# Optimization experiments

Hardware: AMD Instinct MI355X
Metric: run time of the kernel (lower is better)

The kernel has to match this reference:

```python
import jax, jax.numpy as jnp
import numpy as np

B, TX, TY, C, H = 2, 1024, 4096, 768, 12
D = C // H  # head_dim = 64


def setup_inputs() -> dict:
    key = jax.random.key(0)
    ks = jax.random.split(key, 7)
    x = jax.random.normal(ks[0], (B, TX, C), dtype=jnp.float32)
    y = jax.random.normal(ks[1], (B, TY, C), dtype=jnp.float32)
    # sorted float timestamps in [0, TY]
    x_t = jnp.sort(jax.random.uniform(ks[2], (B, TX), dtype=jnp.float32) * TY, axis=-1)
    y_t = jnp.sort(jax.random.uniform(ks[3], (B, TY), dtype=jnp.float32) * TY, axis=-1)
    y_t = y_t.at[:, 0].set(0.0)  # guarantee every query sees >=1 valid key
    Wq = jax.random.normal(ks[4], (C, C), dtype=jnp.float32) * 0.02
    Wkv = jax.random.normal(ks[5], (C, 2 * C), dtype=jnp.float32) * 0.02
    Wproj = jax.random.normal(ks[6], (C, C), dtype=jnp.float32) * 0.02
    # RotaryEmbedding(dim=D, learned_freq=True): init values are the standard inv freqs
    inv_freq = 1.0 / (10000.0 ** (jnp.arange(0, D, 2, dtype=jnp.float32) / D))
    return {"x": x, "x_t": x_t, "y": y, "y_t": y_t, "dist": 512, "min_dist": 0,
            "Wq": Wq, "Wkv": Wkv, "Wproj": Wproj, "inv_freq": inv_freq}


def _rotate_half(t):
    # interleaved pair rotation: (x1, x2) -> (-x2, x1)
    p = t.reshape(t.shape[:-1] + (-1, 2))
    x1, x2 = p[..., 0], p[..., 1]
    return jnp.stack((-x2, x1), axis=-1).reshape(t.shape)


def _apply_rope(t, pos, inv_freq):
    # t: (B,H,T,D), pos: (B,T), inv_freq: (D/2,)
    f = pos[:, None, :, None] * inv_freq          # (B,1,T,D/2)
    f = jnp.repeat(f, 2, axis=-1)                 # (B,1,T,D) interleaved
    return t * jnp.cos(f) + _rotate_half(t) * jnp.sin(f)


def reference(x, x_t, y, y_t, dist, min_dist, Wq, Wkv, Wproj, inv_freq):
    q = (x @ Wq).reshape(B, TX, H, D).transpose(0, 2, 1, 3)   # (B,H,TX,D)
    kv = y @ Wkv
    k = kv[..., :C].reshape(B, TY, H, D).transpose(0, 2, 1, 3)
    v = kv[..., C:].reshape(B, TY, H, D).transpose(0, 2, 1, 3)
    q = _apply_rope(q, x_t, inv_freq)
    k = _apply_rope(k, y_t, inv_freq)
    # time-window mask: valid iff (x_t - min_dist) >= y_t and (x_t - min_dist) <= y_t + dist
    xt = (x_t - min_dist)[:, :, None]             # (B,TX,1)
    yt = y_t[:, None, :]                          # (B,1,TY)
    mask = (xt >= yt) & (xt <= yt + dist)         # (B,TX,TY)
    scores = jnp.einsum('bhqd,bhkd->bhqk', q, k) / jnp.sqrt(jnp.float32(D))
    scores = jnp.where(mask[:, None, :, :], scores, -jnp.inf)
    attn = jax.nn.softmax(scores, axis=-1)
    out = jnp.einsum('bhqk,bhkd->bhqd', attn, v)
    out = out.transpose(0, 2, 1, 3).reshape(B, TX, C)
    return out @ Wproj
```

## Files before the change

### kernel.cpp

```cpp
#include <hip/hip_runtime.h>
#include <hip/hip_bf16.h>
#include <math.h>

#define B_ 2
#define TX_ 1024
#define TY_ 4096
#define C_ 768
#define H_ 12
#define D_ 64
#define NSPLIT 4
#define R_ (B_ * H_ * TX_)

typedef __bf16 bf16x8 __attribute__((ext_vector_type(8)));
typedef float floatx4 __attribute__((ext_vector_type(4)));

__device__ __forceinline__ void async_copy16(const void* g, void* l) {
    __builtin_amdgcn_global_load_lds(
        (const __attribute__((address_space(1))) unsigned int*)g,
        (__attribute__((address_space(3))) unsigned int*)l,
        16, 0, 0);
}

__device__ __forceinline__ bf16x8 cvt8(const float* s) {
    bf16x8 r;
#pragma unroll
    for (int i = 0; i < 8; i++) r[i] = (__bf16)s[i];
    return r;
}

__global__ __launch_bounds__(256)
void prep(const float* __restrict__ x,  __bf16* __restrict__ xb,
          const float* __restrict__ y,  __bf16* __restrict__ yb,
          const float* __restrict__ Wq, __bf16* __restrict__ Wqt,
          const float* __restrict__ Wkv,__bf16* __restrict__ Wkvt,
          const float* __restrict__ Wpr,__bf16* __restrict__ Wprt)
{
    __shared__ float tile[32][33];
    const int bid = blockIdx.x;
    if (bid >= 2304) {
        const int cb = bid - 2304;
        const float* src; __bf16* dst; size_t base;
        if (cb < 768) { src = x; dst = xb; base = (size_t)cb * 2048; }
        else          { src = y; dst = yb; base = (size_t)(cb - 768) * 2048; }
        const size_t i = base + threadIdx.x * 8;
        float4 v0 = *(const float4*)(src + i);
        float4 v1 = *(const float4*)(src + i + 4);
        bf16x8 p;
        p[0] = (__bf16)v0.x; p[1] = (__bf16)v0.y; p[2] = (__bf16)v0.z; p[3] = (__bf16)v0.w;
        p[4] = (__bf16)v1.x; p[5] = (__bf16)v1.y; p[6] = (__bf16)v1.z; p[7] = (__bf16)v1.w;
        *(bf16x8*)(dst + i) = p;
        return;
    }
    const int bxr = bid % 96;
    const int byr = bid / 96;
    const float* W; __bf16* Wt; int N, nb; float scale = 1.0f;
    if (bxr < 24)      { W = Wq;  Wt = Wqt;  N = C_;     nb = bxr;      scale = 0.125f; }
    else if (bxr < 72) { W = Wkv; Wt = Wkvt; N = 2 * C_; nb = bxr - 24; }
    else               { W = Wpr; Wt = Wprt; N = C_;     nb = bxr - 72; }
    const int bx = nb * 32;
    const int by = byr * 32;
    const int tx = threadIdx.x & 31, ty = threadIdx.x >> 5;
#pragma unroll
    for (int i = 0; i < 4; i++)
        tile[ty + i * 8][tx] = W[(size_t)(by + ty + i * 8) * N + bx + tx];
    __syncthreads();
#pragma unroll
    for (int i = 0; i < 4; i++)
        Wt[(size_t)(bx + ty + i * 8) * C_ + by + tx] =
            (__bf16)(tile[tx][ty + i * 8] * scale);
}

__global__ __launch_bounds__(256)
void gemm_qkv(const __bf16* __restrict__ xb, const __bf16* __restrict__ Wqt,
              const __bf16* __restrict__ yb, const __bf16* __restrict__ Wkvt,
              __bf16* __restrict__ Qbh, __bf16* __restrict__ Kbh,
              __bf16* __restrict__ Vtb,
              const float* __restrict__ x_t, const float* __restrict__ y_t,
              const float* __restrict__ inv_freq)
{
    const int bid = blockIdx.x;
    const bool isQ = (bid < 96);
    const __bf16* A; const __bf16* Bt; const float* t_arr;
    int row0, n0, T, TSH;
    if (isQ) {
        A = xb; Bt = Wqt; t_arr = x_t;
        row0 = (bid / 6) * 128; n0 = (bid % 6) * 128; T = TX_; TSH = 10;
    } else {
        const int r = bid - 96;
        A = yb; Bt = Wkvt; t_arr = y_t;
        row0 = (r / 12) * 128; n0 = (r % 12) * 128; T = TY_; TSH = 12;
    }
    const bool isV = (!isQ) && (n0 >= C_);

    __shared__ __align__(16) float smem_f[8192];
    __bf16* smem_b = (__bf16*)smem_f;

    const int tid  = threadIdx.x;
    const int wave = tid >> 6;
    const int lane = tid & 63;
    const int m16  = lane & 15;
    const int quad = lane >> 4;
    const int wm   = wave >> 1;
    const int wn   = wave & 1;

    floatx4 acc[4][4];
#pragma unroll
    for (int i = 0; i < 4; i++)
#pragma unroll
        for (int j = 0; j < 4; j++) acc[i][j] = (floatx4){0.f, 0.f, 0.f, 0.f};

    int srow[4], scol[4];
#pragma unroll
    for (int j = 0; j < 4; j++) {
        int e = j * 2048 + wave * 512 + lane * 8;
        int e2 = e & 4095;
        srow[j] = e2 >> 5;
        scol[j] = e2 & 31;
    }

    for (int k0 = 0; k0 < C_; k0 += 64) {
        __syncthreads();
#pragma unroll
        for (int c = 0; c < 2; c++) {
            const int kk = k0 + c * 32;
#pragma unroll
            for (int j = 0; j < 4; j++) {
                const __bf16* src = (j < 2)
                    ? A  + (size_t)(row0 + srow[j]) * C_ + (kk + scol[j])
                    : Bt + (size_t)(n0   + srow[j]) * C_ + (kk + scol[j]);
                async_copy16(src, (char*)smem_f + c * 16384 + j * 4096 + wave * 1024);
            }
        }
        __syncthreads();

#pragma unroll
        for (int c = 0; c < 2; c++) {
            const __bf16* As = smem_b + c * 8192;
            const __bf16* Bs = As + 4096;
            bf16x8 af[4], bfr[4];
#pragma unroll
            for (int i = 0; i < 4; i++)
                af[i] = *(const bf16x8*)(As + (size_t)(wm * 64 + i * 16 + m16) * 32 + quad * 8);
#pragma unroll
            for (int j = 0; j < 4; j++)
                bfr[j] = *(const bf16x8*)(Bs + (size_t)(wn * 64 + j * 16 + m16) * 32 + quad * 8);
#pragma unroll
            for (int i = 0; i < 4; i++)
#pragma unroll
                for (int j = 0; j < 4; j++)
                    acc[i][j] = __builtin_amdgcn_mfma_f32_16x16x32_bf16(af[i], bfr[j], acc[i][j], 0, 0, 0);
        }
    }

    const int STR = 132;
    float* fs = smem_f;

#pragma unroll
    for (int i = 0; i < 4; i++) {
        __syncthreads();
#pragma unroll
        for (int j = 0; j < 4; j++) {
            const int col_l = wn * 64 + j * 16 + m16;
#pragma unroll
            for (int r = 0; r < 4; r++) {
                const int row_l = quad * 4 + r;
                float v = acc[i][j][r];
                if (!isV) {
                    const float vp = __shfl_xor(v, 1);
                    const int row = row0 + wm * 64 + i * 16 + row_l;
                    const int cc = (n0 + col_l) & (D_ - 1);
                    const float fr = t_arr[row] * inv_freq[cc >> 1];
                    const float sn = __sinf(fr), cs = __cosf(fr);
                    v = (m16 & 1) ? (v * cs + vp * sn) : (v * cs - vp * sn);
                }
                fs[(wm * 16 + row_l) * STR + col_l] = v;
            }
        }
        __syncthreads();

        if (!isV) {
            __bf16* outb = isQ ? Qbh : Kbh;
            const int r32 = tid >> 3;
            const int lane8 = tid & 7;
            const int grow = row0 + (r32 >> 4) * 64 + i * 16 + (r32 & 15);
            const int bb = grow >> TSH;
            const int rk = grow & (T - 1);
            const int h  = (n0 >> 6) + (lane8 >> 2);
            const int d0 = (lane8 & 3) * 16;
            __bf16* gp = outb + ((size_t)(bb * H_ + h) * T + rk) * 64 + d0;
            const float* sp = &fs[r32 * STR + lane8 * 16];
            *(bf16x8*)gp       = cvt8(sp);
            *(bf16x8*)(gp + 8) = cvt8(sp + 8);
        } else {
            const int dcol = tid >> 1;
            const int g16  = tid & 1;
            const int h  = ((n0 - C_) >> 6) + (dcol >> 6);
            const int dd = dcol & 63;
            const int kbase = row0 + g16 * 64 + i * 16;
            const int bb  = kbase >> 12;
            const int kin = kbase & (TY_ - 1);
            float tmp[16];
#pragma unroll
            for (int jj = 0; jj < 16; jj++)
                tmp[jj] = fs[(g16 * 16 + jj) * STR + dcol];
            __bf16* gp = Vtb + ((size_t)(bb * H_ + h) * 64 + dd) * TY_ + kin;
            *(bf16x8*)gp       = cvt8(tmp);
            *(bf16x8*)(gp + 8) = cvt8(tmp + 8);
        }
    }
}

__global__ __launch_bounds__(256)
void attn_mfma(const __bf16* __restrict__ Qb,
               const __bf16* __restrict__ Kb,
               const __bf16* __restrict__ Vt,
               const float* __restrict__ x_t,
               const float* __restrict__ y_t,
               const int* __restrict__ dist_p,
               const int* __restrict__ min_dist_p,
               float* __restrict__ pacc,
               float* __restrict__ pml)
{
    __shared__ __align__(16) __bf16 Kc[64 * 64];
    __shared__ __align__(16) __bf16 Vc[64 * 64];
    __shared__ __align__(16) __bf16 Pt[4][16 * 64];

    const int tid  = threadIdx.x;
    const int wave = tid >> 6;
    const int m16  = tid & 15;
    const int quad = (tid & 63) >> 4;
    const int qt = blockIdx.x, bh = blockIdx.y, split = blockIdx.z;
    const int b = bh / H_;
    const int qblk  = qt * 64;
    const int qbase = qblk + wave * 16;

    const float dist = (float)dist_p[0];
    const float md   = (float)min_dist_p[0];
    const float* yt = y_t + (size_t)b * TY_;
    const float* xt = x_t + (size_t)b * TX_;

    const float xtmin = xt[qblk] - md;
    const float xtmax = xt[qblk + 63] - md;
    int lo = 0, hi = TY_;
    while (lo < hi) { int mid = (lo + hi) >> 1; if (yt[mid] + dist < xtmin) lo = mid + 1; else hi = mid; }
    const int klo = lo;
    lo = 0; hi = TY_;
    while (lo < hi) { int mid = (lo + hi) >> 1; if (yt[mid] <= xtmax) lo = mid + 1; else hi = mid; }
    const int khi = lo - 1;
    const int len = khi - klo + 1;

    int k0 = klo, k1 = klo;
    if (len > 0) {
        const int cnt = (len + NSPLIT - 1) / NSPLIT;
        k0 = klo + split * cnt;
        k1 = min(k0 + cnt, klo + len);
    }

    float xtq[4];
#pragma unroll
    for (int r = 0; r < 4; r++)
        xtq[r] = xt[qbase + quad * 4 + r] - md;

    const __bf16* qp = Qb + ((size_t)bh * TX_ + qbase + m16) * 64;
    const bf16x8 aq0 = *(const bf16x8*)(qp + quad * 8);
    const bf16x8 aq1 = *(const bf16x8*)(qp + 32 + quad * 8);

    float l[4];
    floatx4 o[4];
#pragma unroll
    for (int r = 0; r < 4; r++) l[r] = 0.f;
#pragma unroll
    for (int t = 0; t < 4; t++) o[t] = (floatx4){0.f, 0.f, 0.f, 0.f};

    for (int kc = k0; kc < k1; kc += 64) {
        float ytv[4];
#pragma unroll
        for (int c = 0; c < 4; c++)
            ytv[c] = yt[min(kc + c * 16 + m16, TY_ - 1)];

        __syncthreads();
        {
            const int krow = tid >> 3;
            const int kseg = (tid & 7) * 8;
            async_copy16(Kb + ((size_t)bh * TY_ + min(kc + krow, TY_ - 1)) * 64 + kseg,
                         (char*)Kc + tid * 16);
            async_copy16(Kb + ((size_t)bh * TY_ + min(kc + 32 + krow, TY_ - 1)) * 64 + kseg,
                         (char*)Kc + 4096 + tid * 16);
            const int d   = tid >> 3;
            const int kvs = min(kc + (tid & 7) * 8, TY_ - 8);
            async_copy16(Vt + ((size_t)bh * 64 + d) * TY_ + kvs,
                         (char*)Vc + tid * 16);
            async_copy16(Vt + ((size_t)bh * 64 + 32 + d) * TY_ + kvs,
                         (char*)Vc + 4096 + tid * 16);
        }
        __syncthreads();

        floatx4 s[4];
#pragma unroll
        for (int c = 0; c < 4; c++) {
            const bf16x8 bk0 = *(const bf16x8*)(Kc + (c * 16 + m16) * 64 + quad * 8);
            const bf16x8 bk1 = *(const bf16x8*)(Kc + (c * 16 + m16) * 64 + 32 + quad * 8);
            s[c] = (floatx4){0.f, 0.f, 0.f, 0.f};
            s[c] = __builtin_amdgcn_mfma_f32_16x16x32_bf16(aq0, bk0, s[c], 0, 0, 0);
            s[c] = __builtin_amdgcn_mfma_f32_16x16x32_bf16(aq1, bk1, s[c], 0, 0, 0);
        }

        __bf16* pt = Pt[wave];
#pragma unroll
        for (int r = 0; r < 4; r++) {
#pragma unroll
            for (int c = 0; c < 4; c++) {
                const int kg = kc + c * 16 + m16;
                const bool v = (kg < k1) && (xtq[r] >= ytv[c]) && (xtq[r] <= ytv[c] + dist);
                const float p = v ? (float)(__bf16)__expf(s[c][r]) : 0.f;
                l[r] += p;
                pt[(quad * 4 + r) * 64 + c * 16 + m16] = (__bf16)p;
            }
        }
        const bf16x8 ap0 = *(const bf16x8*)(pt + m16 * 64 + quad * 8);
        const bf16x8 ap1 = *(const bf16x8*)(pt + m16 * 64 + 32 + quad * 8);
#pragma unroll
        for (int t = 0; t < 4; t++) {
            const bf16x8 bv0 = *(const bf16x8*)(Vc + (t * 16 + m16) * 64 + quad * 8);
            const bf16x8 bv1 = *(const bf16x8*)(Vc + (t * 16 + m16) * 64 + 32 + quad * 8);
            o[t] = __builtin_amdgcn_mfma_f32_16x16x32_bf16(ap0, bv0, o[t], 0, 0, 0);
            o[t] = __builtin_amdgcn_mfma_f32_16x16x32_bf16(ap1, bv1, o[t], 0, 0, 0);
        }
    }

#pragma unroll
    for (int r = 0; r < 4; r++) {
#pragma unroll
        for (int w = 1; w < 16; w <<= 1)
            l[r] += __shfl_xor(l[r], w);
    }

#pragma unroll
    for (int t = 0; t < 4; t++)
#pragma unroll
        for (int r = 0; r < 4; r++) {
            const size_t gr = (size_t)bh * TX_ + qbase + quad * 4 + r;
            pacc[((size_t)split * R_ + gr) * 64 + t * 16 + m16] = o[t][r];
        }
    if (m16 == 0) {
#pragma unroll
        for (int r = 0; r < 4; r++) {
            const size_t gr = (size_t)bh * TX_ + qbase + quad * 4 + r;
            pml[(size_t)split * R_ + gr] = l[r];
        }
    }
}

__global__ __launch_bounds__(256)
void combine_kernel(const float* __restrict__ pacc,
                    const float* __restrict__ pml,
                    __bf16* __restrict__ O)
{
    const int d   = threadIdx.x;
    const int sub = threadIdx.y;
    const size_t r = (size_t)blockIdx.x * 4 + sub;
    const int bh  = (int)(r / TX_);
    const int txg = (int)(r % TX_);
    const int b = bh / H_, h = bh % H_;

    float L = 0.f, val = 0.f;
#pragma unroll
    for (int s = 0; s < NSPLIT; s++) {
        L   += pml[(size_t)s * R_ + r];
        val += pacc[((size_t)s * R_ + r) * 64 + d];
    }
    const float o = (L > 0.f) ? val / L : 0.f;
    O[(size_t)(b * TX_ + txg) * C_ + h * D_ + d] = (__bf16)o;
}

__global__ __launch_bounds__(256)
void gemm_proj(const __bf16* __restrict__ A,
               const __bf16* __restrict__ Bt,
               float* __restrict__ out0)
{
    __shared__ __align__(16) float smem_f[8192];
    __bf16* smem_b = (__bf16*)smem_f;

    const int tid  = threadIdx.x;
    const int wave = tid >> 6;
    const int lane = tid & 63;
    const int m16  = lane & 15;
    const int quad = lane >> 4;
    const int wm   = wave >> 1;
    const int wn   = wave & 1;
    const int row0 = blockIdx.y * 128;
    const int n0   = blockIdx.x * 128;

    floatx4 acc[4][4];
#pragma unroll
    for (int i = 0; i < 4; i++)
#pragma unroll
        for (int j = 0; j < 4; j++) acc[i][j] = (floatx4){0.f, 0.f, 0.f, 0.f};

    int srow[4], scol[4];
#pragma unroll
    for (int j = 0; j < 4; j++) {
        int e = j * 2048 + wave * 512 + lane * 8;
        int e2 = e & 4095;
        srow[j] = e2 >> 5;
        scol[j] = e2 & 31;
    }

    for (int k0 = 0; k0 < C_; k0 += 64) {
        __syncthreads();
#pragma unroll
        for (int c = 0; c < 2; c++) {
            const int kk = k0 + c * 32;
#pragma unroll
            for (int j = 0; j < 4; j++) {
                const __bf16* src = (j < 2)
                    ? A  + (size_t)(row0 + srow[j]) * C_ + (kk + scol[j])
                    : Bt + (size_t)(n0   + srow[j]) * C_ + (kk + scol[j]);
                async_copy16(src, (char*)smem_f + c * 16384 + j * 4096 + wave * 1024);
            }
        }
        __syncthreads();

#pragma unroll
        for (int c = 0; c < 2; c++) {
            const __bf16* As = smem_b + c * 8192;
            const __bf16* Bs = As + 4096;
            bf16x8 af[4], bfr[4];
#pragma unroll
            for (int i = 0; i < 4; i++)
                af[i] = *(const bf16x8*)(As + (size_t)(wm * 64 + i * 16 + m16) * 32 + quad * 8);
#pragma unroll
            for (int j = 0; j < 4; j++)
                bfr[j] = *(const bf16x8*)(Bs + (size_t)(wn * 64 + j * 16 + m16) * 32 + quad * 8);
#pragma unroll
            for (int i = 0; i < 4; i++)
#pragma unroll
                for (int j = 0; j < 4; j++)
                    acc[i][j] = __builtin_amdgcn_mfma_f32_16x16x32_bf16(af[i], bfr[j], acc[i][j], 0, 0, 0);
        }
    }

    const int STR = 132;
    float* fs = smem_f;
#pragma unroll
    for (int i = 0; i < 4; i++) {
        __syncthreads();
#pragma unroll
        for (int j = 0; j < 4; j++) {
            const int col_l = wn * 64 + j * 16 + m16;
#pragma unroll
            for (int r = 0; r < 4; r++)
                fs[(wm * 16 + quad * 4 + r) * STR + col_l] = acc[i][j][r];
        }
        __syncthreads();
        const int r32 = tid >> 3;
        const int lc  = (tid & 7) * 4;
        const int row = row0 + (r32 >> 4) * 64 + i * 16 + (r32 & 15);
        float* gp = out0 + (size_t)row * C_ + n0;
#pragma unroll
        for (int c2 = 0; c2 < 4; c2++) {
            float4 v4 = *(const float4*)&fs[r32 * STR + c2 * 32 + lc];
            *(float4*)(gp + c2 * 32 + lc) = v4;
        }
    }
}

extern "C" void kernel_launch(void* const* d_in, const int* in_sizes, int n_in,
                              void* d_out, int out_size, void* d_ws, size_t ws_size,
                              hipStream_t stream)
{
    const float* x        = (const float*)d_in[0];
    const float* x_t      = (const float*)d_in[1];
    const float* y        = (const float*)d_in[2];
    const float* y_t      = (const float*)d_in[3];
    const int*   dist     = (const int*)d_in[4];
    const int*   min_dist = (const int*)d_in[5];
    const float* Wq       = (const float*)d_in[6];
    const float* Wkv      = (const float*)d_in[7];
    const float* Wproj    = (const float*)d_in[8];
    const float* inv_freq = (const float*)d_in[9];
    float* out = (float*)d_out;

    const size_t QN = (size_t)B_ * TX_ * C_;
    const size_t KN = (size_t)B_ * TY_ * C_;

    float* ws = (float*)d_ws;
    float* pacc = ws; ws += (size_t)NSPLIT * R_ * 64;
    float* pml  = ws; ws += (size_t)NSPLIT * R_;
    __bf16* bws = (__bf16*)ws;
    __bf16* xb    = bws; bws += QN;
    __bf16* yb    = bws; bws += KN;
    __bf16* Wqt   = bws; bws += (size_t)C_ * C_;
    __bf16* Wkvt  = bws; bws += (size_t)C_ * 2 * C_;
    __bf16* Wprt  = bws; bws += (size_t)C_ * C_;
    __bf16* Ob    = bws; bws += QN;
    __bf16* Qbh   = bws; bws += QN;
    __bf16* Kbh   = bws; bws += KN;
    __bf16* Vtb   = bws; bws += KN;

    prep<<<dim3(2304 + 3840), dim3(256), 0, stream>>>(
        x, xb, y, yb, Wq, Wqt, Wkv, Wkvt, Wproj, Wprt);

    gemm_qkv<<<dim3(864), dim3(256), 0, stream>>>(
        xb, Wqt, yb, Wkvt, Qbh, Kbh, Vtb, x_t, y_t, inv_freq);

    attn_mfma<<<dim3(TX_ / 64, B_ * H_, NSPLIT), dim3(256), 0, stream>>>(
        Qbh, Kbh, Vtb, x_t, y_t, dist, min_dist, pacc, pml);

    combine_kernel<<<dim3((unsigned)(R_ / 4)), dim3(64, 4), 0, stream>>>(
        pacc, pml, Ob);

    gemm_proj<<<dim3(C_ / 128, (B_ * TX_) / 128), dim3(256), 0, stream>>>(
        Ob, Wprt, out);
}
```

Before: 210.6 us.

## Load K/V fragments directly from global memory and use per-wave key ranges

Removes the shared-memory K and V staging tiles and the two block-wide barriers per key chunk; each wave now loads its MFMA K and V operands directly from global memory. The valid key window is computed per wave from its own 16 queries instead of per 64-query block, so waves skip chunks outside their narrower window. The cost is that the four waves no longer share K/V loads, so global/L2 traffic rises and operands are no longer prefetched asynchronously. V reads near the end of the buffer may go past TY, so the workspace is padded.

```diff
diff --git a/kernel.cpp b/kernel.cpp
--- a/kernel.cpp
+++ b/kernel.cpp
@@ -221,8 +221,6 @@
                float* __restrict__ pacc,
                float* __restrict__ pml)
 {
-    __shared__ __align__(16) __bf16 Kc[64 * 64];
-    __shared__ __align__(16) __bf16 Vc[64 * 64];
     __shared__ __align__(16) __bf16 Pt[4][16 * 64];
 
     const int tid  = threadIdx.x;
@@ -231,21 +229,20 @@
     const int quad = (tid & 63) >> 4;
     const int qt = blockIdx.x, bh = blockIdx.y, split = blockIdx.z;
     const int b = bh / H_;
-    const int qblk  = qt * 64;
-    const int qbase = qblk + wave * 16;
+    const int qbase = qt * 64 + wave * 16;
 
     const float dist = (float)dist_p[0];
     const float md   = (float)min_dist_p[0];
     const float* yt = y_t + (size_t)b * TY_;
     const float* xt = x_t + (size_t)b * TX_;
 
-    const float xtmin = xt[qblk] - md;
-    const float xtmax = xt[qblk + 63] - md;
+    const float xtlo = xt[qbase] - md;
+    const float xthi = xt[qbase + 15] - md;
     int lo = 0, hi = TY_;
-    while (lo < hi) { int mid = (lo + hi) >> 1; if (yt[mid] + dist < xtmin) lo = mid + 1; else hi = mid; }
+    while (lo < hi) { int mid = (lo + hi) >> 1; if (yt[mid] + dist < xtlo) lo = mid + 1; else hi = mid; }
     const int klo = lo;
     lo = 0; hi = TY_;
-    while (lo < hi) { int mid = (lo + hi) >> 1; if (yt[mid] <= xtmax) lo = mid + 1; else hi = mid; }
+    while (lo < hi) { int mid = (lo + hi) >> 1; if (yt[mid] <= xthi) lo = mid + 1; else hi = mid; }
     const int khi = lo - 1;
     const int len = khi - klo + 1;
 
@@ -265,6 +262,9 @@
     const bf16x8 aq0 = *(const bf16x8*)(qp + quad * 8);
     const bf16x8 aq1 = *(const bf16x8*)(qp + 32 + quad * 8);
 
+    const __bf16* kbase_p = Kb + (size_t)bh * TY_ * 64;
+    const __bf16* vbase_p = Vt + (size_t)bh * 64 * TY_;
+
     float l[4];
     floatx4 o[4];
 #pragma unroll
@@ -272,57 +272,42 @@
 #pragma unroll
     for (int t = 0; t < 4; t++) o[t] = (floatx4){0.f, 0.f, 0.f, 0.f};
 
+    __bf16* pt = Pt[wave];
+
     for (int kc = k0; kc < k1; kc += 64) {
+        floatx4 s[4];
         float ytv[4];
 #pragma unroll
-        for (int c = 0; c < 4; c++)
-            ytv[c] = yt[min(kc + c * 16 + m16, TY_ - 1)];
-
-        __syncthreads();
-        {
-            const int krow = tid >> 3;
-            const int kseg = (tid & 7) * 8;
-            async_copy16(Kb + ((size_t)bh * TY_ + min(kc + krow, TY_ - 1)) * 64 + kseg,
-                         (char*)Kc + tid * 16);
-            async_copy16(Kb + ((size_t)bh * TY_ + min(kc + 32 + krow, TY_ - 1)) * 64 + kseg,
-                         (char*)Kc + 4096 + tid * 16);
-            const int d   = tid >> 3;
-            const int kvs = min(kc + (tid & 7) * 8, TY_ - 8);
-            async_copy16(Vt + ((size_t)bh * 64 + d) * TY_ + kvs,
-                         (char*)Vc + tid * 16);
-            async_copy16(Vt + ((size_t)bh * 64 + 32 + d) * TY_ + kvs,
-                         (char*)Vc + 4096 + tid * 16);
-        }
-        __syncthreads();
-
-        floatx4 s[4];
-#pragma unroll
         for (int c = 0; c < 4; c++) {
-            const bf16x8 bk0 = *(const bf16x8*)(Kc + (c * 16 + m16) * 64 + quad * 8);
-            const bf16x8 bk1 = *(const bf16x8*)(Kc + (c * 16 + m16) * 64 + 32 + quad * 8);
+            const int kg = min(kc + c * 16 + m16, TY_ - 1);
+            ytv[c] = yt[kg];
+            const __bf16* kp = kbase_p + (size_t)kg * 64;
+            const bf16x8 bk0 = *(const bf16x8*)(kp + quad * 8);
+            const bf16x8 bk1 = *(const bf16x8*)(kp + 32 + quad * 8);
             s[c] = (floatx4){0.f, 0.f, 0.f, 0.f};
             s[c] = __builtin_amdgcn_mfma_f32_16x16x32_bf16(aq0, bk0, s[c], 0, 0, 0);
             s[c] = __builtin_amdgcn_mfma_f32_16x16x32_bf16(aq1, bk1, s[c], 0, 0, 0);
         }
 
-        __bf16* pt = Pt[wave];
 #pragma unroll
         for (int r = 0; r < 4; r++) {
 #pragma unroll
             for (int c = 0; c < 4; c++) {
                 const int kg = kc + c * 16 + m16;
                 const bool v = (kg < k1) && (xtq[r] >= ytv[c]) && (xtq[r] <= ytv[c] + dist);
-                const float p = v ? (float)(__bf16)__expf(s[c][r]) : 0.f;
-                l[r] += p;
-                pt[(quad * 4 + r) * 64 + c * 16 + m16] = (__bf16)p;
+                const __bf16 pb = v ? (__bf16)__expf(s[c][r]) : (__bf16)0.f;
+                l[r] += (float)pb;
+                pt[(quad * 4 + r) * 64 + c * 16 + m16] = pb;
             }
         }
         const bf16x8 ap0 = *(const bf16x8*)(pt + m16 * 64 + quad * 8);
         const bf16x8 ap1 = *(const bf16x8*)(pt + m16 * 64 + 32 + quad * 8);
+
 #pragma unroll
         for (int t = 0; t < 4; t++) {
-            const bf16x8 bv0 = *(const bf16x8*)(Vc + (t * 16 + m16) * 64 + quad * 8);
-            const bf16x8 bv1 = *(const bf16x8*)(Vc + (t * 16 + m16) * 64 + 32 + quad * 8);
+            const __bf16* vp = vbase_p + (size_t)(t * 16 + m16) * TY_;
+            const bf16x8 bv0 = *(const bf16x8*)(vp + kc + quad * 8);
+            const bf16x8 bv1 = *(const bf16x8*)(vp + kc + 32 + quad * 8);
             o[t] = __builtin_amdgcn_mfma_f32_16x16x32_bf16(ap0, bv0, o[t], 0, 0, 0);
             o[t] = __builtin_amdgcn_mfma_f32_16x16x32_bf16(ap1, bv1, o[t], 0, 0, 0);
         }
@@ -496,7 +481,7 @@
     __bf16* Ob    = bws; bws += QN;
     __bf16* Qbh   = bws; bws += QN;
     __bf16* Kbh   = bws; bws += KN;
-    __bf16* Vtb   = bws; bws += KN;
+    __bf16* Vtb   = bws; bws += KN + 128;
 
     prep<<<dim3(2304 + 3840), dim3(256), 0, stream>>>(
         x, xb, y, yb, Wq, Wqt, Wkv, Wkvt, Wproj, Wprt);
```

Result: slower. 258.1 us (+22.6%).
